# Optimization experiments

Hardware: AMD Instinct MI355X
Metric: run time of the kernel (lower is better)

## Reference

```python
import jax, jax.numpy as jnp
import numpy as np
import itertools

N_OBJECTS = 6  # subsets of range(6), sizes 1..6 -> 63 subsets

def _subset_groups():
    # group subsets by length so each group runs as one batched LSTM
    groups = {}
    for m in range(1, N_OBJECTS + 1):
        for s in itertools.combinations(range(6), m):
            groups.setdefault(m, []).append(list(s))
    return [(m, np.asarray(v, dtype=np.int32)) for m, v in groups.items()]

SUBSET_GROUPS = _subset_groups()


def _lstm_final_h(x, W_ih, W_hh, b_ih, b_hh):
    """x: [B,T,D] -> final hidden state [B,H]. PyTorch gate order i,f,g,o."""
    H = W_hh.shape[1]
    B = x.shape[0]
    # precompute input projections for all timesteps: [B,T,4H]
    xz = jnp.einsum('btd,gd->btg', x, W_ih) + b_ih + b_hh

    def step(carry, xt):
        h, c = carry
        z = xt + h @ W_hh.T
        i, f, g, o = jnp.split(z, 4, axis=-1)
        c = jax.nn.sigmoid(f) * c + jax.nn.sigmoid(i) * jnp.tanh(g)
        h = jax.nn.sigmoid(o) * jnp.tanh(c)
        return (h, c), None

    h0 = jnp.zeros((B, H), x.dtype)
    (h, _), _ = jax.lax.scan(step, (h0, h0), jnp.swapaxes(xz, 0, 1))
    return h


def setup_inputs() -> dict:
    key = jax.random.key(0)
    ks = jax.random.split(key, 10)
    D, H, FC, A = 16, 128, 256, 10
    mb = 8192
    s = lambda k, shape, fan: jax.random.normal(k, shape, jnp.float32) * (1.0 / np.sqrt(fan))
    return {
        'x_input': jax.random.normal(ks[0], (mb, 6, D), jnp.float32),
        'W_ih': s(ks[1], (4 * H, D), D),
        'W_hh': s(ks[2], (4 * H, H), H),
        'b_ih': jnp.zeros((4 * H,), jnp.float32),
        'b_hh': jnp.zeros((4 * H,), jnp.float32),
        'fc1_W': s(ks[3], (FC, H), H),
        'fc1_b': jnp.zeros((FC,), jnp.float32),
        'fc2_W': s(ks[4], (A, FC), FC),
        'fc2_b': jnp.zeros((A,), jnp.float32),
    }


def reference(x_input, W_ih, W_hh, b_ih, b_hh, fc1_W, fc1_b, fc2_W, fc2_b):
    mb = x_input.shape[0]
    H = W_hh.shape[1]
    hs = []
    # subsets of the same length are batched into one LSTM pass (fused form of
    # the original 63-iteration python loop); aggregation is permutation-invariant
    for m, idx in SUBSET_GROUPS:
        nL = idx.shape[0]
        xg = x_input[:, idx, :]                       # [mb, nL, m, D] gather
        xg = xg.reshape(mb * nL, m, x_input.shape[-1])
        h = _lstm_final_h(xg, W_ih, W_hh, b_ih, b_hh)  # [mb*nL, H]
        hs.append(h.reshape(mb, nL, H))
    holder = jnp.concatenate(hs, axis=1)              # [mb, 63, H]
    x = jnp.max(holder, axis=1)                       # aggregate == 'max'
    x = jax.nn.relu(x @ fc1_W.T + fc1_b)
    x = x @ fc2_W.T + fc2_b
    return jax.nn.log_softmax(x, axis=-1)
```

## Files before the change

### kernel.cpp

```cpp
#include <hip/hip_runtime.h>
#include <hip/hip_bf16.h>

#define BLOCK   512
#define NSAMP   16
#define HDIM    128
#define DDIM    16
#define NOBJ    6
#define NSLOT   17

typedef __attribute__((ext_vector_type(8))) short bf16x8;
typedef __attribute__((ext_vector_type(4))) float f32x4;

constexpr int pc6(int m)  { int c = 0; for (int i = 0; i < 6; ++i) c += (m >> i) & 1; return c; }
constexpr int msb6(int m) { int b = -1; for (int i = 0; i < 6; ++i) if (m & (1 << i)) b = i; return b; }

struct GChild { int jo, sl; bool bar; };
struct Plan3 {
    int    gps [32];
    int    gbeg[33];
    GChild ch  [63];
    int    lvlG[8];
    bool   ok;
};
constexpr Plan3 make_plan3() {
    Plan3 P{};
    P.ok = true;
    int  slotOf[64] = {};
    bool busy[NSLOT] = {};
    int  pendingFree[NSLOT] = {};
    int  npend = 0;
    int  g = 0, cidx = 0;
    for (int d = 1; d <= 6; ++d) {
        P.lvlG[d] = g;
        for (int Pm = 0; Pm < 64; ++Pm) {
            if (pc6(Pm) != d - 1) continue;
            if (Pm != 0 && msb6(Pm) == 5) continue;
            P.gps[g]  = (Pm == 0) ? -1 : slotOf[Pm];
            P.gbeg[g] = cidx;
            if (Pm != 0) pendingFree[npend++] = slotOf[Pm];
            const int j0 = (Pm == 0) ? 0 : msb6(Pm) + 1;
            for (int j = j0; j <= 5; ++j) {
                const int M = Pm | (1 << j);
                P.ch[cidx].jo  = j;
                P.ch[cidx].bar = false;
                int sl = -1;
                if (j < 5) {
                    int fs = -1;
                    for (int s = 0; s < NSLOT; ++s) if (!busy[s]) { fs = s; break; }
                    if (fs < 0) {
                        P.ch[cidx].bar = true;
                        for (int i = 0; i < npend; ++i) busy[pendingFree[i]] = false;
                        npend = 0;
                        for (int s = 0; s < NSLOT; ++s) if (!busy[s]) { fs = s; break; }
                        if (fs < 0) P.ok = false;
                    }
                    if (fs >= 0) { busy[fs] = true; slotOf[M] = fs; sl = fs; }
                }
                P.ch[cidx].sl = sl;
                ++cidx;
            }
            ++g;
        }
        for (int i = 0; i < npend; ++i) busy[pendingFree[i]] = false;
        npend = 0;
    }
    P.lvlG[7] = g;
    P.gbeg[g] = cidx;
    if (g != 32 || cidx != 63) P.ok = false;
    return P;
}
constexpr Plan3 PL3 = make_plan3();
static_assert(PL3.ok, "plan allocation failed");
static_assert(PL3.lvlG[7] == 32, "32 groups expected");
static_assert(PL3.gbeg[32] == 63, "63 children expected");

#define LOG2E   1.44269504f
#define TWOL2E  2.88539008f
#define SLOT_SH 2048

__device__ __forceinline__ unsigned short f2bf(float x) {
    union { float f; unsigned int u; } a; a.f = x;
    unsigned int r = (a.u + 0x7FFFu + ((a.u >> 16) & 1u)) >> 16;
    return (unsigned short)r;
}
__device__ __forceinline__ unsigned pk2(float a, float b) {
    union { __hip_bfloat162 h; unsigned u; } z;
    z.h = __float22bfloat162_rn(float2{a, b});
    return z.u;
}
__device__ __forceinline__ float bflo(unsigned p) {
    union { unsigned u; float f; } a; a.u = p << 16; return a.f;
}
__device__ __forceinline__ float bfhi(unsigned p) {
    union { unsigned u; float f; } a; a.u = p & 0xFFFF0000u; return a.f;
}


__global__ __launch_bounds__(BLOCK)
__attribute__((amdgpu_waves_per_eu(2, 4)))
void subset_lstm_skew_kernel(
    const float* __restrict__ x_input,
    const float* __restrict__ W_ih,
    const float* __restrict__ W_hh,
    const float* __restrict__ b_ih,
    const float* __restrict__ b_hh,
    const float* __restrict__ fc1_W,
    const float* __restrict__ fc1_b,
    const float* __restrict__ fc2_W,
    const float* __restrict__ fc2_b,
    float* __restrict__ out)
{
    __shared__ __align__(16) unsigned short hs [NSLOT * SLOT_SH];
    __shared__ __align__(16) unsigned short csb[NSLOT * SLOT_SH];
    __shared__ __align__(16) unsigned short xb[NOBJ * 4 * NSAMP * 8];
    float* s_maxh  = (float*)hs;
    float* s_fc1   = (float*)(hs + 4096);
    float* s_logit = (float*)xb;

    const int t      = threadIdx.x;
    const int w      = t >> 6;
    const int lane   = t & 63;
    const int quad   = lane >> 4;
    const int m16    = lane & 15;
    const int s_base = blockIdx.x * NSAMP;

    for (int idx = t; idx < NOBJ * 4 * NSAMP * 8; idx += BLOCK) {
        const int j = idx & 7, n = (idx >> 3) & 15, q = (idx >> 7) & 3, obj = idx >> 9;
        float v;
        if (q < 2) v = x_input[(s_base + n) * (NOBJ * DDIM) + obj * DDIM + q * 8 + j];
        else       v = (q == 2 && j == 0) ? 1.0f : 0.0f;
        xb[idx] = f2bf(v);
    }

    bf16x8 wf[4][5];
    #pragma unroll
    for (int g = 0; g < 4; ++g) {
        const float sc = (g == 2) ? TWOL2E : -LOG2E;
        const int grow = g * HDIM + w * 16 + m16;
        const float* whr = W_hh + grow * HDIM;
        const float* wir = W_ih + grow * DDIM;
        #pragma unroll
        for (int q = 0; q < 4; ++q) {
            union { unsigned short u[8]; bf16x8 v; } pk;
            #pragma unroll
            for (int j = 0; j < 8; ++j)
                pk.u[j] = f2bf(sc * whr[q * 32 + quad * 8 + j]);
            wf[g][q] = pk.v;
        }
        {
            union { unsigned short u[8]; bf16x8 v; } pk;
            #pragma unroll
            for (int j = 0; j < 8; ++j) {
                float v = 0.0f;
                if (quad < 2) v = sc * wir[quad * 8 + j];
                else if (quad == 2 && j == 0) v = sc * (b_ih[grow] + b_hh[grow]);
                pk.u[j] = f2bf(v);
            }
            wf[g][4] = pk.v;
        }
    }

    float mh[4] = {-1e30f, -1e30f, -1e30f, -1e30f};
    const int kslot = w * 2 + (quad >> 1);
    unsigned short* const c_lane = &csb[(((w * 4 + quad) * NSAMP) + m16) * 4];

    auto pointwise_node = [&](const f32x4 (&acc)[4], uint2 cpk, int sl) {
        float cn4[4], hn4[4];
        #pragma unroll
        for (int r = 0; r < 4; ++r) {
            const unsigned p = (r < 2) ? cpk.x : cpk.y;
            const float cprev = (r & 1) ? bfhi(p) : bflo(p);
            const float u  = 1.0f + __builtin_amdgcn_exp2f(acc[0][r]);
            const float q  = 1.0f + __builtin_amdgcn_exp2f(acc[1][r]);
            const float v  = 1.0f + __builtin_amdgcn_exp2f(acc[2][r]);
            const float qo = 1.0f + __builtin_amdgcn_exp2f(acc[3][r]);
            const float uv  = u * v;
            const float num = fmaf(q, v - 2.0f, cprev * uv);
            const float cn  = num * __builtin_amdgcn_rcpf(q * uv);
            const float wt  = 1.0f + __builtin_amdgcn_exp2f(TWOL2E * cn);
            const float h   = (wt - 2.0f) * __builtin_amdgcn_rcpf(qo * wt);
            cn4[r] = cn; hn4[r] = h;
            mh[r] = fmaxf(mh[r], h);
        }
        if (sl >= 0) {
            uint2 cw; cw.x = pk2(cn4[0], cn4[1]); cw.y = pk2(cn4[2], cn4[3]);
            *(uint2*)(c_lane + sl * SLOT_SH) = cw;
            uint2 hw; hw.x = pk2(hn4[0], hn4[1]); hw.y = pk2(hn4[2], hn4[3]);
            *(uint2*)&hs[((sl * 16 + kslot) * NSAMP + m16) * 8 + (quad & 1) * 4] = hw;
        }
    };

    #pragma unroll
    for (int d = 1; d <= 6; ++d) {
        __syncthreads();
        const int gBeg = PL3.lvlG[d];
        const int gEnd = PL3.lvlG[d + 1];
        #pragma unroll
        for (int gi = gBeg; gi < gEnd; ++gi) {
            const int ps = PL3.gps[gi];
            f32x4 zh[4];
            uint2 cpkP; cpkP.x = 0u; cpkP.y = 0u;
            #pragma unroll
            for (int g2 = 0; g2 < 4; ++g2) zh[g2] = f32x4{0.f, 0.f, 0.f, 0.f};
            if (ps >= 0) {
                cpkP = *(const uint2*)(c_lane + ps * SLOT_SH);
                #pragma unroll
                for (int q = 0; q < 4; ++q) {
                    const bf16x8 bh = *(const bf16x8*)
                        &hs[((ps * 16 + q * 4 + quad) * NSAMP + m16) * 8];
                    #pragma unroll
                    for (int g2 = 0; g2 < 4; ++g2)
                        zh[g2] = __builtin_amdgcn_mfma_f32_16x16x32_bf16(
                            wf[g2][q], bh, zh[g2], 0, 0, 0);
                }
            }
            #pragma unroll
            for (int ci = PL3.gbeg[gi]; ci < PL3.gbeg[gi + 1]; ++ci) {
                if (PL3.ch[ci].bar) __syncthreads();
                const bf16x8 bfx = *(const bf16x8*)
                    &xb[((PL3.ch[ci].jo * 4 + quad) * NSAMP + m16) * 8];
                f32x4 acc[4];
                #pragma unroll
                for (int g2 = 0; g2 < 4; ++g2)
                    acc[g2] = __builtin_amdgcn_mfma_f32_16x16x32_bf16(
                        wf[g2][4], bfx, zh[g2], 0, 0, 0);
                pointwise_node(acc, cpkP, PL3.ch[ci].sl);
            }
        }
    }

    __syncthreads();
    {
        float4 v; v.x = mh[0]; v.y = mh[1]; v.z = mh[2]; v.w = mh[3];
        *(float4*)&s_maxh[m16 * HDIM + w * 16 + quad * 4] = v;
    }
    __syncthreads();

    {
        const int f  = t & 255;
        const int sh = t >> 8;
        float a1[8];
        #pragma unroll
        for (int s = 0; s < 8; ++s) a1[s] = fc1_b[f];
        for (int k4 = 0; k4 < HDIM / 4; ++k4) {
            const float4 wv = *(const float4*)&fc1_W[f * HDIM + k4 * 4];
            #pragma unroll
            for (int s = 0; s < 8; ++s) {
                const float4 h4 = *(const float4*)&s_maxh[(sh * 8 + s) * HDIM + k4 * 4];
                a1[s] += wv.x * h4.x + wv.y * h4.y + wv.z * h4.z + wv.w * h4.w;
            }
        }
        #pragma unroll
        for (int s = 0; s < 8; ++s)
            s_fc1[(sh * 8 + s) * 256 + f] = fmaxf(a1[s], 0.0f);
    }
    __syncthreads();

    if (t < NSAMP * 10) {
        const int s = t / 10, a = t % 10;
        float acc2 = fc2_b[a];
        for (int f4 = 0; f4 < 256 / 4; ++f4) {
            const float4 wv = *(const float4*)&fc2_W[a * 256 + f4 * 4];
            const float4 v  = *(const float4*)&s_fc1[s * 256 + f4 * 4];
            acc2 += wv.x * v.x + wv.y * v.y + wv.z * v.z + wv.w * v.w;
        }
        s_logit[s * 10 + a] = acc2;
    }
    __syncthreads();

    if (t < NSAMP) {
        float m = -1e30f;
        #pragma unroll
        for (int a = 0; a < 10; ++a) m = fmaxf(m, s_logit[t * 10 + a]);
        float sum = 0.0f;
        #pragma unroll
        for (int a = 0; a < 10; ++a) sum += __expf(s_logit[t * 10 + a] - m);
        const float lse = m + __logf(sum);
        #pragma unroll
        for (int a = 0; a < 10; ++a)
            out[(s_base + t) * 10 + a] = s_logit[t * 10 + a] - lse;
    }
}

extern "C" void kernel_launch(void* const* d_in, const int* in_sizes, int n_in,
                              void* d_out, int out_size, void* d_ws, size_t ws_size,
                              hipStream_t stream)
{
    (void)d_ws; (void)ws_size; (void)n_in; (void)out_size;

    const float* x   = (const float*)d_in[0];
    const float* Wih = (const float*)d_in[1];
    const float* Whh = (const float*)d_in[2];
    const float* bih = (const float*)d_in[3];
    const float* bhh = (const float*)d_in[4];
    const float* f1w = (const float*)d_in[5];
    const float* f1b = (const float*)d_in[6];
    const float* f2w = (const float*)d_in[7];
    const float* f2b = (const float*)d_in[8];

    const int mb = in_sizes[0] / (NOBJ * DDIM);
    dim3 grid(mb / NSAMP), block(BLOCK);
    subset_lstm_skew_kernel<<<grid, block, 0, stream>>>(
        x, Wih, Whh, bih, bhh, f1w, f1b, f2w, f2b, (float*)d_out);
}
```

Measured before the change: 190.8 us.

## Factor gate exponentials and keep cell state in registers instead of LDS

Uses exp(a+b)=exp(a)*exp(b) to precompute exponentials of the input projections for objects 3-5 once into shared memory. Children on those objects then skip the input MFMA and the four per-gate exp2 calls, doing one exp over the parent hidden projection per group and an FMA per child. The cell state now lives in a per-thread register array instead of a bf16 LDS buffer, and the slot count drops from 17 to 14 to fit the new LDS table. The trade-offs are higher register pressure, possible overflow in the exp product, and more barriers from the smaller slot pool.

```diff
diff --git a/kernel.cpp b/kernel.cpp
--- a/kernel.cpp
+++ b/kernel.cpp
@@ -6,7 +6,7 @@
 #define HDIM    128
 #define DDIM    16
 #define NOBJ    6
-#define NSLOT   17
+#define NSLOT   14
 
 typedef __attribute__((ext_vector_type(8))) short bf16x8;
 typedef __attribute__((ext_vector_type(4))) float f32x4;
@@ -49,6 +49,7 @@
                     for (int s = 0; s < NSLOT; ++s) if (!busy[s]) { fs = s; break; }
                     if (fs < 0) {
                         P.ch[cidx].bar = true;
+                        if (npend == 0) P.ok = false;
                         for (int i = 0; i < npend; ++i) busy[pendingFree[i]] = false;
                         npend = 0;
                         for (int s = 0; s < NSLOT; ++s) if (!busy[s]) { fs = s; break; }
@@ -87,12 +88,6 @@
     union { __hip_bfloat162 h; unsigned u; } z;
     z.h = __float22bfloat162_rn(float2{a, b});
     return z.u;
-}
-__device__ __forceinline__ float bflo(unsigned p) {
-    union { unsigned u; float f; } a; a.u = p << 16; return a.f;
-}
-__device__ __forceinline__ float bfhi(unsigned p) {
-    union { unsigned u; float f; } a; a.u = p & 0xFFFF0000u; return a.f;
 }
 
 
@@ -111,7 +106,7 @@
     float* __restrict__ out)
 {
     __shared__ __align__(16) unsigned short hs [NSLOT * SLOT_SH];
-    __shared__ __align__(16) unsigned short csb[NSLOT * SLOT_SH];
+    __shared__ __align__(16) float          Exs[3 * 4 * 8 * 64 * 4];
     __shared__ __align__(16) unsigned short xb[NOBJ * 4 * NSAMP * 8];
     float* s_maxh  = (float*)hs;
     float* s_fc1   = (float*)(hs + 4096);
@@ -160,31 +155,44 @@
         }
     }
 
+    __syncthreads();
+
+    #pragma unroll
+    for (int j3 = 0; j3 < 3; ++j3) {
+        const bf16x8 bfx = *(const bf16x8*)&xb[(((j3 + 3) * 4 + quad) * NSAMP + m16) * 8];
+        #pragma unroll
+        for (int g = 0; g < 4; ++g) {
+            const f32x4 a = __builtin_amdgcn_mfma_f32_16x16x32_bf16(
+                wf[g][4], bfx, f32x4{0.f, 0.f, 0.f, 0.f}, 0, 0, 0);
+            float4 e;
+            e.x = __builtin_amdgcn_exp2f(a[0]);
+            e.y = __builtin_amdgcn_exp2f(a[1]);
+            e.z = __builtin_amdgcn_exp2f(a[2]);
+            e.w = __builtin_amdgcn_exp2f(a[3]);
+            *(float4*)&Exs[((((j3 * 4 + g) * 8 + w) * 64) + quad * 16 + m16) * 4] = e;
+        }
+    }
+
     float mh[4] = {-1e30f, -1e30f, -1e30f, -1e30f};
     const int kslot = w * 2 + (quad >> 1);
-    unsigned short* const c_lane = &csb[(((w * 4 + quad) * NSAMP) + m16) * 4];
-
-    auto pointwise_node = [&](const f32x4 (&acc)[4], uint2 cpk, int sl) {
-        float cn4[4], hn4[4];
+    float c_slots[NSLOT][4];
+
+    auto pw_tail = [&](const float (&u4)[4], const float (&q4)[4],
+                       const float (&v4)[4], const float (&qo4)[4],
+                       const float (&cp4)[4], int sl) {
+        float hn4[4];
         #pragma unroll
         for (int r = 0; r < 4; ++r) {
-            const unsigned p = (r < 2) ? cpk.x : cpk.y;
-            const float cprev = (r & 1) ? bfhi(p) : bflo(p);
-            const float u  = 1.0f + __builtin_amdgcn_exp2f(acc[0][r]);
-            const float q  = 1.0f + __builtin_amdgcn_exp2f(acc[1][r]);
-            const float v  = 1.0f + __builtin_amdgcn_exp2f(acc[2][r]);
-            const float qo = 1.0f + __builtin_amdgcn_exp2f(acc[3][r]);
-            const float uv  = u * v;
-            const float num = fmaf(q, v - 2.0f, cprev * uv);
-            const float cn  = num * __builtin_amdgcn_rcpf(q * uv);
+            const float uv  = u4[r] * v4[r];
+            const float num = fmaf(q4[r], v4[r] - 2.0f, cp4[r] * uv);
+            const float cn  = num * __builtin_amdgcn_rcpf(q4[r] * uv);
             const float wt  = 1.0f + __builtin_amdgcn_exp2f(TWOL2E * cn);
-            const float h   = (wt - 2.0f) * __builtin_amdgcn_rcpf(qo * wt);
-            cn4[r] = cn; hn4[r] = h;
+            const float h   = (wt - 2.0f) * __builtin_amdgcn_rcpf(qo4[r] * wt);
+            hn4[r] = h;
             mh[r] = fmaxf(mh[r], h);
+            if (sl >= 0) c_slots[sl][r] = cn;
         }
         if (sl >= 0) {
-            uint2 cw; cw.x = pk2(cn4[0], cn4[1]); cw.y = pk2(cn4[2], cn4[3]);
-            *(uint2*)(c_lane + sl * SLOT_SH) = cw;
             uint2 hw; hw.x = pk2(hn4[0], hn4[1]); hw.y = pk2(hn4[2], hn4[3]);
             *(uint2*)&hs[((sl * 16 + kslot) * NSAMP + m16) * 8 + (quad & 1) * 4] = hw;
         }
@@ -199,11 +207,11 @@
         for (int gi = gBeg; gi < gEnd; ++gi) {
             const int ps = PL3.gps[gi];
             f32x4 zh[4];
-            uint2 cpkP; cpkP.x = 0u; cpkP.y = 0u;
+            float Eh[4][4];
+            float cp4[4];
             #pragma unroll
             for (int g2 = 0; g2 < 4; ++g2) zh[g2] = f32x4{0.f, 0.f, 0.f, 0.f};
             if (ps >= 0) {
-                cpkP = *(const uint2*)(c_lane + ps * SLOT_SH);
                 #pragma unroll
                 for (int q = 0; q < 4; ++q) {
                     const bf16x8 bh = *(const bf16x8*)
@@ -213,18 +221,64 @@
                         zh[g2] = __builtin_amdgcn_mfma_f32_16x16x32_bf16(
                             wf[g2][q], bh, zh[g2], 0, 0, 0);
                 }
+                #pragma unroll
+                for (int g2 = 0; g2 < 4; ++g2)
+                    #pragma unroll
+                    for (int r = 0; r < 4; ++r)
+                        Eh[g2][r] = __builtin_amdgcn_exp2f(zh[g2][r]);
+                #pragma unroll
+                for (int r = 0; r < 4; ++r) cp4[r] = c_slots[ps][r];
+            } else {
+                #pragma unroll
+                for (int g2 = 0; g2 < 4; ++g2)
+                    #pragma unroll
+                    for (int r = 0; r < 4; ++r) Eh[g2][r] = 1.0f;
+                #pragma unroll
+                for (int r = 0; r < 4; ++r) cp4[r] = 0.0f;
             }
             #pragma unroll
             for (int ci = PL3.gbeg[gi]; ci < PL3.gbeg[gi + 1]; ++ci) {
                 if (PL3.ch[ci].bar) __syncthreads();
-                const bf16x8 bfx = *(const bf16x8*)
-                    &xb[((PL3.ch[ci].jo * 4 + quad) * NSAMP + m16) * 8];
-                f32x4 acc[4];
-                #pragma unroll
-                for (int g2 = 0; g2 < 4; ++g2)
-                    acc[g2] = __builtin_amdgcn_mfma_f32_16x16x32_bf16(
-                        wf[g2][4], bfx, zh[g2], 0, 0, 0);
-                pointwise_node(acc, cpkP, PL3.ch[ci].sl);
+                const int jo = PL3.ch[ci].jo;
+                float u4[4], q4[4], v4[4], qo4[4];
+                if (jo >= 3) {
+                    const int j3 = jo - 3;
+                    const float4 e0 = *(const float4*)
+                        &Exs[((((j3 * 4 + 0) * 8 + w) * 64) + quad * 16 + m16) * 4];
+                    const float4 e1 = *(const float4*)
+                        &Exs[((((j3 * 4 + 1) * 8 + w) * 64) + quad * 16 + m16) * 4];
+                    const float4 e2 = *(const float4*)
+                        &Exs[((((j3 * 4 + 2) * 8 + w) * 64) + quad * 16 + m16) * 4];
+                    const float4 e3 = *(const float4*)
+                        &Exs[((((j3 * 4 + 3) * 8 + w) * 64) + quad * 16 + m16) * 4];
+                    const float ex0[4] = {e0.x, e0.y, e0.z, e0.w};
+                    const float ex1[4] = {e1.x, e1.y, e1.z, e1.w};
+                    const float ex2[4] = {e2.x, e2.y, e2.z, e2.w};
+                    const float ex3[4] = {e3.x, e3.y, e3.z, e3.w};
+                    #pragma unroll
+                    for (int r = 0; r < 4; ++r) {
+                        u4[r]  = fmaf(Eh[0][r], ex0[r], 1.0f);
+                        q4[r]  = fmaf(Eh[1][r], ex1[r], 1.0f);
+                        v4[r]  = fmaf(Eh[2][r], ex2[r], 1.0f);
+                        qo4[r] = fmaf(Eh[3][r], ex3[r], 1.0f);
+                    }
+                } else {
+                    const bf16x8 bfx = *(const bf16x8*)
+                        &xb[((jo * 4 + quad) * NSAMP + m16) * 8];
+                    f32x4 acc[4];
+                    #pragma unroll
+                    for (int g2 = 0; g2 < 4; ++g2)
+                        acc[g2] = __builtin_amdgcn_mfma_f32_16x16x32_bf16(
+                            wf[g2][4], bfx, zh[g2], 0, 0, 0);
+                    #pragma unroll
+                    for (int r = 0; r < 4; ++r) {
+                        u4[r]  = 1.0f + __builtin_amdgcn_exp2f(acc[0][r]);
+                        q4[r]  = 1.0f + __builtin_amdgcn_exp2f(acc[1][r]);
+                        v4[r]  = 1.0f + __builtin_amdgcn_exp2f(acc[2][r]);
+                        qo4[r] = 1.0f + __builtin_amdgcn_exp2f(acc[3][r]);
+                    }
+                }
+                pw_tail(u4, q4, v4, qo4, cp4, PL3.ch[ci].sl);
             }
         }
     }
```

New measurement: 190.4 us. No clear change (-0.2%).

## Process two sample tiles per block and keep cell state in registers

Applied to the files above, without the earlier changes.

Each block now handles two 16-sample tiles, so the register-resident gate weights are reused across twice as many MFMA columns and the number of blocks is halved. The cell-state buffer in shared memory is removed and replaced by a per-lane register array of packed bf16 cell values indexed by slot. NSLOT drops to 14 to fit the larger hidden-state buffers. In exchange, register pressure rises (c_pk alone is 56 VGPRs), which can lower occupancy or cause spills, and there are half as many blocks to spread across CUs.

```diff
diff --git a/kernel.cpp b/kernel.cpp
--- a/kernel.cpp
+++ b/kernel.cpp
@@ -3,10 +3,11 @@
 
 #define BLOCK   512
 #define NSAMP   16
+#define NTILE   2
 #define HDIM    128
 #define DDIM    16
 #define NOBJ    6
-#define NSLOT   17
+#define NSLOT   14
 
 typedef __attribute__((ext_vector_type(8))) short bf16x8;
 typedef __attribute__((ext_vector_type(4))) float f32x4;
@@ -49,6 +50,7 @@
                     for (int s = 0; s < NSLOT; ++s) if (!busy[s]) { fs = s; break; }
                     if (fs < 0) {
                         P.ch[cidx].bar = true;
+                        if (npend == 0) P.ok = false;
                         for (int i = 0; i < npend; ++i) busy[pendingFree[i]] = false;
                         npend = 0;
                         for (int s = 0; s < NSLOT; ++s) if (!busy[s]) { fs = s; break; }
@@ -76,7 +78,7 @@
 
 #define LOG2E   1.44269504f
 #define TWOL2E  2.88539008f
-#define SLOT_SH 2048
+#define SLOT_SH (16 * NTILE * NSAMP * 8)
 
 __device__ __forceinline__ unsigned short f2bf(float x) {
     union { float f; unsigned int u; } a; a.f = x;
@@ -110,11 +112,10 @@
     const float* __restrict__ fc2_b,
     float* __restrict__ out)
 {
-    __shared__ __align__(16) unsigned short hs [NSLOT * SLOT_SH];
-    __shared__ __align__(16) unsigned short csb[NSLOT * SLOT_SH];
-    __shared__ __align__(16) unsigned short xb[NOBJ * 4 * NSAMP * 8];
+    __shared__ __align__(16) unsigned short hs[NSLOT * SLOT_SH];
+    __shared__ __align__(16) unsigned short xb[NOBJ * 4 * NTILE * NSAMP * 8];
     float* s_maxh  = (float*)hs;
-    float* s_fc1   = (float*)(hs + 4096);
+    float* s_fc1   = (float*)(hs + 8192);
     float* s_logit = (float*)xb;
 
     const int t      = threadIdx.x;
@@ -122,12 +123,12 @@
     const int lane   = t & 63;
     const int quad   = lane >> 4;
     const int m16    = lane & 15;
-    const int s_base = blockIdx.x * NSAMP;
-
-    for (int idx = t; idx < NOBJ * 4 * NSAMP * 8; idx += BLOCK) {
-        const int j = idx & 7, n = (idx >> 3) & 15, q = (idx >> 7) & 3, obj = idx >> 9;
+    const int s_base = blockIdx.x * (NTILE * NSAMP);
+
+    for (int idx = t; idx < NOBJ * 4 * NTILE * NSAMP * 8; idx += BLOCK) {
+        const int j = idx & 7, n5 = (idx >> 3) & 31, q = (idx >> 8) & 3, obj = idx >> 10;
         float v;
-        if (q < 2) v = x_input[(s_base + n) * (NOBJ * DDIM) + obj * DDIM + q * 8 + j];
+        if (q < 2) v = x_input[(s_base + n5) * (NOBJ * DDIM) + obj * DDIM + q * 8 + j];
         else       v = (q == 2 && j == 0) ? 1.0f : 0.0f;
         xb[idx] = f2bf(v);
     }
@@ -160,33 +161,36 @@
         }
     }
 
-    float mh[4] = {-1e30f, -1e30f, -1e30f, -1e30f};
+    float mh[NTILE][4];
+    #pragma unroll
+    for (int tl = 0; tl < NTILE; ++tl)
+        #pragma unroll
+        for (int r = 0; r < 4; ++r) mh[tl][r] = -1e30f;
     const int kslot = w * 2 + (quad >> 1);
-    unsigned short* const c_lane = &csb[(((w * 4 + quad) * NSAMP) + m16) * 4];
-
-    auto pointwise_node = [&](const f32x4 (&acc)[4], uint2 cpk, int sl) {
+    uint2 c_pk[NTILE][NSLOT];
+
+    auto pw_tail = [&](int tl, const f32x4 (&acc)[4], const float (&cp4)[4], int sl) {
         float cn4[4], hn4[4];
         #pragma unroll
         for (int r = 0; r < 4; ++r) {
-            const unsigned p = (r < 2) ? cpk.x : cpk.y;
-            const float cprev = (r & 1) ? bfhi(p) : bflo(p);
             const float u  = 1.0f + __builtin_amdgcn_exp2f(acc[0][r]);
             const float q  = 1.0f + __builtin_amdgcn_exp2f(acc[1][r]);
             const float v  = 1.0f + __builtin_amdgcn_exp2f(acc[2][r]);
             const float qo = 1.0f + __builtin_amdgcn_exp2f(acc[3][r]);
             const float uv  = u * v;
-            const float num = fmaf(q, v - 2.0f, cprev * uv);
+            const float num = fmaf(q, v - 2.0f, cp4[r] * uv);
             const float cn  = num * __builtin_amdgcn_rcpf(q * uv);
             const float wt  = 1.0f + __builtin_amdgcn_exp2f(TWOL2E * cn);
             const float h   = (wt - 2.0f) * __builtin_amdgcn_rcpf(qo * wt);
             cn4[r] = cn; hn4[r] = h;
-            mh[r] = fmaxf(mh[r], h);
+            mh[tl][r] = fmaxf(mh[tl][r], h);
         }
         if (sl >= 0) {
-            uint2 cw; cw.x = pk2(cn4[0], cn4[1]); cw.y = pk2(cn4[2], cn4[3]);
-            *(uint2*)(c_lane + sl * SLOT_SH) = cw;
+            c_pk[tl][sl].x = pk2(cn4[0], cn4[1]);
+            c_pk[tl][sl].y = pk2(cn4[2], cn4[3]);
             uint2 hw; hw.x = pk2(hn4[0], hn4[1]); hw.y = pk2(hn4[2], hn4[3]);
-            *(uint2*)&hs[((sl * 16 + kslot) * NSAMP + m16) * 8 + (quad & 1) * 4] = hw;
+            *(uint2*)&hs[((sl * 16 + kslot) * (NTILE * NSAMP) + tl * NSAMP + m16) * 8
+                         + (quad & 1) * 4] = hw;
         }
     };
 
@@ -198,65 +202,90 @@
         #pragma unroll
         for (int gi = gBeg; gi < gEnd; ++gi) {
             const int ps = PL3.gps[gi];
-            f32x4 zh[4];
-            uint2 cpkP; cpkP.x = 0u; cpkP.y = 0u;
-            #pragma unroll
-            for (int g2 = 0; g2 < 4; ++g2) zh[g2] = f32x4{0.f, 0.f, 0.f, 0.f};
+            f32x4 zh[NTILE][4];
+            float cp4[NTILE][4];
+            #pragma unroll
+            for (int tl = 0; tl < NTILE; ++tl)
+                #pragma unroll
+                for (int g2 = 0; g2 < 4; ++g2) zh[tl][g2] = f32x4{0.f, 0.f, 0.f, 0.f};
             if (ps >= 0) {
-                cpkP = *(const uint2*)(c_lane + ps * SLOT_SH);
                 #pragma unroll
                 for (int q = 0; q < 4; ++q) {
-                    const bf16x8 bh = *(const bf16x8*)
-                        &hs[((ps * 16 + q * 4 + quad) * NSAMP + m16) * 8];
+                    #pragma unroll
+                    for (int tl = 0; tl < NTILE; ++tl) {
+                        const bf16x8 bh = *(const bf16x8*)
+                            &hs[((ps * 16 + q * 4 + quad) * (NTILE * NSAMP)
+                                 + tl * NSAMP + m16) * 8];
+                        #pragma unroll
+                        for (int g2 = 0; g2 < 4; ++g2)
+                            zh[tl][g2] = __builtin_amdgcn_mfma_f32_16x16x32_bf16(
+                                wf[g2][q], bh, zh[tl][g2], 0, 0, 0);
+                    }
+                }
+                #pragma unroll
+                for (int tl = 0; tl < NTILE; ++tl) {
+                    cp4[tl][0] = bflo(c_pk[tl][ps].x);
+                    cp4[tl][1] = bfhi(c_pk[tl][ps].x);
+                    cp4[tl][2] = bflo(c_pk[tl][ps].y);
+                    cp4[tl][3] = bfhi(c_pk[tl][ps].y);
+                }
+            } else {
+                #pragma unroll
+                for (int tl = 0; tl < NTILE; ++tl)
+                    #pragma unroll
+                    for (int r = 0; r < 4; ++r) cp4[tl][r] = 0.0f;
+            }
+            #pragma unroll
+            for (int ci = PL3.gbeg[gi]; ci < PL3.gbeg[gi + 1]; ++ci) {
+                if (PL3.ch[ci].bar) __syncthreads();
+                const int jo = PL3.ch[ci].jo;
+                const int sl = PL3.ch[ci].sl;
+                f32x4 acc[NTILE][4];
+                #pragma unroll
+                for (int tl = 0; tl < NTILE; ++tl) {
+                    const bf16x8 bfx = *(const bf16x8*)
+                        &xb[((jo * 4 + quad) * (NTILE * NSAMP) + tl * NSAMP + m16) * 8];
                     #pragma unroll
                     for (int g2 = 0; g2 < 4; ++g2)
-                        zh[g2] = __builtin_amdgcn_mfma_f32_16x16x32_bf16(
-                            wf[g2][q], bh, zh[g2], 0, 0, 0);
+                        acc[tl][g2] = __builtin_amdgcn_mfma_f32_16x16x32_bf16(
+                            wf[g2][4], bfx, zh[tl][g2], 0, 0, 0);
                 }
-            }
-            #pragma unroll
-            for (int ci = PL3.gbeg[gi]; ci < PL3.gbeg[gi + 1]; ++ci) {
-                if (PL3.ch[ci].bar) __syncthreads();
-                const bf16x8 bfx = *(const bf16x8*)
-                    &xb[((PL3.ch[ci].jo * 4 + quad) * NSAMP + m16) * 8];
-                f32x4 acc[4];
-                #pragma unroll
-                for (int g2 = 0; g2 < 4; ++g2)
-                    acc[g2] = __builtin_amdgcn_mfma_f32_16x16x32_bf16(
-                        wf[g2][4], bfx, zh[g2], 0, 0, 0);
-                pointwise_node(acc, cpkP, PL3.ch[ci].sl);
+                #pragma unroll
+                for (int tl = 0; tl < NTILE; ++tl)
+                    pw_tail(tl, acc[tl], cp4[tl], sl);
             }
         }
     }
 
     __syncthreads();
-    {
-        float4 v; v.x = mh[0]; v.y = mh[1]; v.z = mh[2]; v.w = mh[3];
-        *(float4*)&s_maxh[m16 * HDIM + w * 16 + quad * 4] = v;
+    #pragma unroll
+    for (int tl = 0; tl < NTILE; ++tl) {
+        float4 v; v.x = mh[tl][0]; v.y = mh[tl][1]; v.z = mh[tl][2]; v.w = mh[tl][3];
+        *(float4*)&s_maxh[(tl * NSAMP + m16) * HDIM + w * 16 + quad * 4] = v;
     }
     __syncthreads();
 
     {
         const int f  = t & 255;
         const int sh = t >> 8;
-        float a1[8];
-        #pragma unroll
-        for (int s = 0; s < 8; ++s) a1[s] = fc1_b[f];
+        float a1[16];
+        #pragma unroll
+        for (int s = 0; s < 16; ++s) a1[s] = fc1_b[f];
         for (int k4 = 0; k4 < HDIM / 4; ++k4) {
             const float4 wv = *(const float4*)&fc1_W[f * HDIM + k4 * 4];
             #pragma unroll
-            for (int s = 0; s < 8; ++s) {
-                const float4 h4 = *(const float4*)&s_maxh[(sh * 8 + s) * HDIM + k4 * 4];
+            for (int s = 0; s < 16; ++s) {
+                const float4 h4 = *(const float4*)&s_maxh[(sh * 16 + s) * HDIM + k4 * 4];
                 a1[s] += wv.x * h4.x + wv.y * h4.y + wv.z * h4.z + wv.w * h4.w;
             }
         }
         #pragma unroll
-        for (int s = 0; s < 8; ++s)
-            s_fc1[(sh * 8 + s) * 256 + f] = fmaxf(a1[s], 0.0f);
+        for (int s = 0; s < 16; ++s)
+            s_fc1[(sh * 16 + s) * 256 + f] = fmaxf(a1[s], 0.0f);
     }
     __syncthreads();
 
-    if (t < NSAMP * 10) {
+    if (t < NTILE * NSAMP * 10) {
         const int s = t / 10, a = t % 10;
         float acc2 = fc2_b[a];
         for (int f4 = 0; f4 < 256 / 4; ++f4) {
@@ -268,7 +297,7 @@
     }
     __syncthreads();
 
-    if (t < NSAMP) {
+    if (t < NTILE * NSAMP) {
         float m = -1e30f;
         #pragma unroll
         for (int a = 0; a < 10; ++a) m = fmaxf(m, s_logit[t * 10 + a]);
@@ -299,7 +328,7 @@
     const float* f2b = (const float*)d_in[8];
 
     const int mb = in_sizes[0] / (NOBJ * DDIM);
-    dim3 grid(mb / NSAMP), block(BLOCK);
+    dim3 grid(mb / (NTILE * NSAMP)), block(BLOCK);
     subset_lstm_skew_kernel<<<grid, block, 0, stream>>>(
         x, Wih, Whh, bih, bhh, f1w, f1b, f2w, f2b, (float*)d_out);
 }
```

After: 188.9 us. About the same (-1.0%).

## Replace fully unrolled subset tree walk with table-driven runtime loop and fewer slots

Applied to the files above, without the earlier changes.

The compile-time unrolled traversal of the 63-node subset tree becomes a rolled loop that reads its schedule (parent slot, child object, target slot, barrier flags) from a device-constant table. The slot count drops from 17 to 14, and a guard rejects plans that would need a barrier with nothing to free. The c-state address is simplified to index by thread id. The aim is smaller code and less LDS use, which may allow more resident blocks. In exchange it adds scalar table loads, loop overhead and possibly extra barriers.

```diff
diff --git a/kernel.cpp b/kernel.cpp
--- a/kernel.cpp
+++ b/kernel.cpp
@@ -6,7 +6,7 @@
 #define HDIM    128
 #define DDIM    16
 #define NOBJ    6
-#define NSLOT   17
+#define NSLOT   14
 
 typedef __attribute__((ext_vector_type(8))) short bf16x8;
 typedef __attribute__((ext_vector_type(4))) float f32x4;
@@ -49,6 +49,7 @@
                     for (int s = 0; s < NSLOT; ++s) if (!busy[s]) { fs = s; break; }
                     if (fs < 0) {
                         P.ch[cidx].bar = true;
+                        if (npend == 0) P.ok = false;
                         for (int i = 0; i < npend; ++i) busy[pendingFree[i]] = false;
                         npend = 0;
                         for (int s = 0; s < NSLOT; ++s) if (!busy[s]) { fs = s; break; }
@@ -73,6 +74,28 @@
 static_assert(PL3.ok, "plan allocation failed");
 static_assert(PL3.lvlG[7] == 32, "32 groups expected");
 static_assert(PL3.gbeg[32] == 63, "63 children expected");
+
+struct PlanRT {
+    int           gps [32];
+    int           gbeg[33];
+    unsigned char gbar[32];
+    unsigned char cjo [63];
+    signed char   csl [63];
+    unsigned char cbar[63];
+};
+constexpr PlanRT make_rt() {
+    PlanRT R{};
+    for (int i = 0; i < 32; ++i) { R.gps[i] = PL3.gps[i]; R.gbar[i] = 0; }
+    for (int i = 0; i < 33; ++i) R.gbeg[i] = PL3.gbeg[i];
+    for (int d = 1; d <= 6; ++d) R.gbar[PL3.lvlG[d]] = 1;
+    for (int i = 0; i < 63; ++i) {
+        R.cjo[i]  = (unsigned char)PL3.ch[i].jo;
+        R.csl[i]  = (signed char)PL3.ch[i].sl;
+        R.cbar[i] = PL3.ch[i].bar ? 1 : 0;
+    }
+    return R;
+}
+__device__ const PlanRT DPL = make_rt();
 
 #define LOG2E   1.44269504f
 #define TWOL2E  2.88539008f
@@ -162,69 +185,67 @@
 
     float mh[4] = {-1e30f, -1e30f, -1e30f, -1e30f};
     const int kslot = w * 2 + (quad >> 1);
-    unsigned short* const c_lane = &csb[(((w * 4 + quad) * NSAMP) + m16) * 4];
-
-    auto pointwise_node = [&](const f32x4 (&acc)[4], uint2 cpk, int sl) {
-        float cn4[4], hn4[4];
-        #pragma unroll
-        for (int r = 0; r < 4; ++r) {
-            const unsigned p = (r < 2) ? cpk.x : cpk.y;
-            const float cprev = (r & 1) ? bfhi(p) : bflo(p);
-            const float u  = 1.0f + __builtin_amdgcn_exp2f(acc[0][r]);
-            const float q  = 1.0f + __builtin_amdgcn_exp2f(acc[1][r]);
-            const float v  = 1.0f + __builtin_amdgcn_exp2f(acc[2][r]);
-            const float qo = 1.0f + __builtin_amdgcn_exp2f(acc[3][r]);
-            const float uv  = u * v;
-            const float num = fmaf(q, v - 2.0f, cprev * uv);
-            const float cn  = num * __builtin_amdgcn_rcpf(q * uv);
-            const float wt  = 1.0f + __builtin_amdgcn_exp2f(TWOL2E * cn);
-            const float h   = (wt - 2.0f) * __builtin_amdgcn_rcpf(qo * wt);
-            cn4[r] = cn; hn4[r] = h;
-            mh[r] = fmaxf(mh[r], h);
-        }
-        if (sl >= 0) {
-            uint2 cw; cw.x = pk2(cn4[0], cn4[1]); cw.y = pk2(cn4[2], cn4[3]);
-            *(uint2*)(c_lane + sl * SLOT_SH) = cw;
-            uint2 hw; hw.x = pk2(hn4[0], hn4[1]); hw.y = pk2(hn4[2], hn4[3]);
-            *(uint2*)&hs[((sl * 16 + kslot) * NSAMP + m16) * 8 + (quad & 1) * 4] = hw;
-        }
-    };
-
-    #pragma unroll
-    for (int d = 1; d <= 6; ++d) {
-        __syncthreads();
-        const int gBeg = PL3.lvlG[d];
-        const int gEnd = PL3.lvlG[d + 1];
-        #pragma unroll
-        for (int gi = gBeg; gi < gEnd; ++gi) {
-            const int ps = PL3.gps[gi];
-            f32x4 zh[4];
-            uint2 cpkP; cpkP.x = 0u; cpkP.y = 0u;
-            #pragma unroll
-            for (int g2 = 0; g2 < 4; ++g2) zh[g2] = f32x4{0.f, 0.f, 0.f, 0.f};
-            if (ps >= 0) {
-                cpkP = *(const uint2*)(c_lane + ps * SLOT_SH);
-                #pragma unroll
-                for (int q = 0; q < 4; ++q) {
-                    const bf16x8 bh = *(const bf16x8*)
-                        &hs[((ps * 16 + q * 4 + quad) * NSAMP + m16) * 8];
-                    #pragma unroll
-                    for (int g2 = 0; g2 < 4; ++g2)
-                        zh[g2] = __builtin_amdgcn_mfma_f32_16x16x32_bf16(
-                            wf[g2][q], bh, zh[g2], 0, 0, 0);
-                }
-            }
-            #pragma unroll
-            for (int ci = PL3.gbeg[gi]; ci < PL3.gbeg[gi + 1]; ++ci) {
-                if (PL3.ch[ci].bar) __syncthreads();
-                const bf16x8 bfx = *(const bf16x8*)
-                    &xb[((PL3.ch[ci].jo * 4 + quad) * NSAMP + m16) * 8];
-                f32x4 acc[4];
+    unsigned short* const c_lane = &csb[t * 4];
+
+    #pragma unroll 1
+    for (int gi = 0; gi < 32; ++gi) {
+        if (DPL.gbar[gi]) __syncthreads();
+        const int ps = DPL.gps[gi];
+        f32x4 zh[4];
+        float cp4[4];
+        #pragma unroll
+        for (int g2 = 0; g2 < 4; ++g2) zh[g2] = f32x4{0.f, 0.f, 0.f, 0.f};
+        if (ps >= 0) {
+            const uint2 cpk = *(const uint2*)(c_lane + ps * SLOT_SH);
+            cp4[0] = bflo(cpk.x); cp4[1] = bfhi(cpk.x);
+            cp4[2] = bflo(cpk.y); cp4[3] = bfhi(cpk.y);
+            #pragma unroll
+            for (int q = 0; q < 4; ++q) {
+                const bf16x8 bh = *(const bf16x8*)
+                    &hs[((ps * 16 + q * 4 + quad) * NSAMP + m16) * 8];
                 #pragma unroll
                 for (int g2 = 0; g2 < 4; ++g2)
-                    acc[g2] = __builtin_amdgcn_mfma_f32_16x16x32_bf16(
-                        wf[g2][4], bfx, zh[g2], 0, 0, 0);
-                pointwise_node(acc, cpkP, PL3.ch[ci].sl);
+                    zh[g2] = __builtin_amdgcn_mfma_f32_16x16x32_bf16(
+                        wf[g2][q], bh, zh[g2], 0, 0, 0);
+            }
+        } else {
+            #pragma unroll
+            for (int r = 0; r < 4; ++r) cp4[r] = 0.0f;
+        }
+        const int cB = DPL.gbeg[gi];
+        const int cE = DPL.gbeg[gi + 1];
+        #pragma unroll 1
+        for (int ci = cB; ci < cE; ++ci) {
+            if (DPL.cbar[ci]) __syncthreads();
+            const int jo = DPL.cjo[ci];
+            const int sl = DPL.csl[ci];
+            const bf16x8 bfx = *(const bf16x8*)
+                &xb[((jo * 4 + quad) * NSAMP + m16) * 8];
+            f32x4 acc[4];
+            #pragma unroll
+            for (int g2 = 0; g2 < 4; ++g2)
+                acc[g2] = __builtin_amdgcn_mfma_f32_16x16x32_bf16(
+                    wf[g2][4], bfx, zh[g2], 0, 0, 0);
+            float cn4[4], hn4[4];
+            #pragma unroll
+            for (int r = 0; r < 4; ++r) {
+                const float u  = 1.0f + __builtin_amdgcn_exp2f(acc[0][r]);
+                const float q  = 1.0f + __builtin_amdgcn_exp2f(acc[1][r]);
+                const float v  = 1.0f + __builtin_amdgcn_exp2f(acc[2][r]);
+                const float qo = 1.0f + __builtin_amdgcn_exp2f(acc[3][r]);
+                const float uv  = u * v;
+                const float num = fmaf(q, v - 2.0f, cp4[r] * uv);
+                const float cn  = num * __builtin_amdgcn_rcpf(q * uv);
+                const float wt  = 1.0f + __builtin_amdgcn_exp2f(TWOL2E * cn);
+                const float h   = (wt - 2.0f) * __builtin_amdgcn_rcpf(qo * wt);
+                cn4[r] = cn; hn4[r] = h;
+                mh[r] = fmaxf(mh[r], h);
+            }
+            if (sl >= 0) {
+                uint2 cw; cw.x = pk2(cn4[0], cn4[1]); cw.y = pk2(cn4[2], cn4[3]);
+                *(uint2*)(c_lane + sl * SLOT_SH) = cw;
+                uint2 hw; hw.x = pk2(hn4[0], hn4[1]); hw.y = pk2(hn4[2], hn4[3]);
+                *(uint2*)&hs[((sl * 16 + kslot) * NSAMP + m16) * 8 + (quad & 1) * 4] = hw;
             }
         }
     }
```

Result: slower. 222.4 us (+16.5%).
